# Kernel optimization log

Hardware: AMD Instinct MI355X
Metric: run time of the kernel (lower is better)

Reference implementation:

```python
import jax, jax.numpy as jnp
import numpy as np

N_HEADS = 8
N_LSTM_LAYERS = 32
HID = 25  # LSTM hidden units == decoder seq_len
EPS = 1e-5


def _layernorm(x, g, b):
    m = x.mean(-1, keepdims=True)
    v = x.var(-1, keepdims=True)  # biased, as torch LayerNorm
    return (x - m) / jnp.sqrt(v + EPS) * g + b


def _mha(q_in, k_in, v_in, Wq, bq, Wk, bk, Wv, bv, Wo, bo):
    B, L, D = q_in.shape
    S = k_in.shape[1]
    E = D // N_HEADS
    q = (q_in @ Wq + bq).reshape(B, L, N_HEADS, E)
    k = (k_in @ Wk + bk).reshape(B, S, N_HEADS, E)
    v = (v_in @ Wv + bv).reshape(B, S, N_HEADS, E)
    scores = jnp.einsum('blhe,bshe->bhls', q, k) / jnp.sqrt(jnp.asarray(E, q.dtype))
    attn = jax.nn.softmax(scores, axis=-1)
    out = jnp.einsum('bhls,bshe->blhe', attn, v).reshape(B, L, D)
    return out @ Wo + bo


def _lstm_layer(inp, W_ih, W_hh, b_ih, b_hh):
    # inp: [B, T, F]; PyTorch gate order i, f, g, o
    B = inp.shape[0]
    h0 = jnp.zeros((B, HID), inp.dtype)
    c0 = jnp.zeros((B, HID), inp.dtype)
    bias = b_ih + b_hh

    def step(carry, x_t):
        h, c = carry
        gates = x_t @ W_ih.T + h @ W_hh.T + bias  # [B, 4H]
        i, f, g, o = jnp.split(gates, 4, axis=-1)
        c = jax.nn.sigmoid(f) * c + jax.nn.sigmoid(i) * jnp.tanh(g)
        h = jax.nn.sigmoid(o) * jnp.tanh(c)
        return (h, c), h

    xs = jnp.swapaxes(inp, 0, 1)  # [T, B, F]
    _, hs = jax.lax.scan(step, (h0, c0), xs)
    return jnp.swapaxes(hs, 0, 1)  # [B, T, H]


def _forward(x, cross,
             Wq_s, bq_s, Wk_s, bk_s, Wv_s, bv_s, Wo_s, bo_s,
             Wq_c, bq_c, Wk_c, bk_c, Wv_c, bv_c, Wo_c, bo_c,
             g1, b1, g2, b2, g3, b3,
             W_ih, W_hh, b_ih, b_hh, Wc, bc):
    x = x + _mha(x, x, x, Wq_s, bq_s, Wk_s, bk_s, Wv_s, bv_s, Wo_s, bo_s)
    x = _layernorm(x, g1, b1)
    x = x + _mha(x, cross, cross, Wq_c, bq_c, Wk_c, bk_c, Wv_c, bv_c, Wo_c, bo_c)
    x = _layernorm(x, g2, b2)
    # LSTM runs over the feature axis: [B, L=25, D=512] -> [B, T=512, F=25]
    y = jnp.swapaxes(x, 1, 2)
    for l in range(N_LSTM_LAYERS):
        y = _lstm_layer(y, W_ih[l], W_hh[l], b_ih[l], b_hh[l])
    # pointwise conv over channels (dim 1 of [B, 512, 25])
    final_y = jnp.einsum('oc,bcl->bol', Wc, y) + bc[None, :, None]
    final_y = jnp.swapaxes(final_y, 1, 2)  # [B, 25, 512]
    return _layernorm(x + final_y, g3, b3)


def setup_inputs() -> dict:
    key = jax.random.key(0)
    ks = jax.random.split(key, 24)
    B, L, S, D = 128, 25, 96, 512

    def rn(k, shape, scale=0.02):
        return jax.random.normal(k, shape, jnp.float32) * scale

    inp = {
        'x': jax.random.normal(ks[0], (B, L, D), jnp.float32),
        'cross': jax.random.normal(ks[1], (B, S, D), jnp.float32),
        'Wq_s': rn(ks[2], (D, D)), 'bq_s': jnp.zeros(D),
        'Wk_s': rn(ks[3], (D, D)), 'bk_s': jnp.zeros(D),
        'Wv_s': rn(ks[4], (D, D)), 'bv_s': jnp.zeros(D),
        'Wo_s': rn(ks[5], (D, D)), 'bo_s': jnp.zeros(D),
        'Wq_c': rn(ks[6], (D, D)), 'bq_c': jnp.zeros(D),
        'Wk_c': rn(ks[7], (D, D)), 'bk_c': jnp.zeros(D),
        'Wv_c': rn(ks[8], (D, D)), 'bv_c': jnp.zeros(D),
        'Wo_c': rn(ks[9], (D, D)), 'bo_c': jnp.zeros(D),
        'g1': jnp.ones(D), 'b1': jnp.zeros(D),
        'g2': jnp.ones(D), 'b2': jnp.zeros(D),
        'g3': jnp.ones(D), 'b3': jnp.zeros(D),
        'W_ih': rn(ks[10], (N_LSTM_LAYERS, 4 * HID, HID), 0.1),
        'W_hh': rn(ks[11], (N_LSTM_LAYERS, 4 * HID, HID), 0.1),
        'b_ih': jnp.zeros((N_LSTM_LAYERS, 4 * HID)),
        'b_hh': jnp.zeros((N_LSTM_LAYERS, 4 * HID)),
        'Wc': rn(ks[12], (D, D)), 'bc': jnp.zeros(D),
    }
    return inp


def reference(x, cross,
              Wq_s, bq_s, Wk_s, bk_s, Wv_s, bv_s, Wo_s, bo_s,
              Wq_c, bq_c, Wk_c, bk_c, Wv_c, bv_c, Wo_c, bo_c,
              g1, b1, g2, b2, g3, b3,
              W_ih, W_hh, b_ih, b_hh, Wc, bc):
    return _forward(x, cross,
                    Wq_s, bq_s, Wk_s, bk_s, Wv_s, bv_s, Wo_s, bo_s,
                    Wq_c, bq_c, Wk_c, bk_c, Wv_c, bv_c, Wo_c, bo_c,
                    g1, b1, g2, b2, g3, b3,
                    W_ih, W_hh, b_ih, b_hh, Wc, bc)
```

## Files before the change

kernel.cpp:

```cpp
#include <hip/hip_runtime.h>


#define EPS_LN 1e-5f

typedef _Float16 h2v __attribute__((ext_vector_type(2)));
typedef _Float16 h8v __attribute__((ext_vector_type(8)));
typedef float    f4v __attribute__((ext_vector_type(4)));

#if defined(__has_builtin)
#if __has_builtin(__builtin_amdgcn_fdot2)
#define HAVE_FDOT2 1
#endif
#endif

__device__ __forceinline__ float fdot2(h2v a, h2v b, float c) {
#ifdef HAVE_FDOT2
  return __builtin_amdgcn_fdot2(a, b, c, false);
#else
  return c + (float)a.x * (float)b.x + (float)a.y * (float)b.y;
#endif
}
__device__ __forceinline__ h2v bch2(unsigned int u) {
  return __builtin_bit_cast(h2v, u);
}

struct WPtrs { const float* p[9]; };

__global__ __launch_bounds__(256)
void prep_weights(WPtrs w, _Float16* __restrict__ dst) {
  __shared__ float tile[32][33];
  const int z = blockIdx.z;
  const int tx = threadIdx.x & 31, ty = threadIdx.x >> 5;
  const int bx = blockIdx.x, by = blockIdx.y;
  const float* in = w.p[z];
  _Float16* outp = dst + (size_t)z * 262144;
  if (z < 8) {
#pragma unroll
    for (int i = 0; i < 4; i++)
      tile[ty + i * 8][tx] = in[(size_t)(by * 32 + ty + i * 8) * 512 + bx * 32 + tx];
    __syncthreads();
#pragma unroll
    for (int i = 0; i < 4; i++)
      outp[(size_t)(bx * 32 + ty + i * 8) * 512 + by * 32 + tx] = (_Float16)tile[tx][ty + i * 8];
  } else {
#pragma unroll
    for (int i = 0; i < 4; i++) {
      size_t off = (size_t)(by * 32 + ty + i * 8) * 512 + bx * 32 + tx;
      outp[off] = (_Float16)in[off];
    }
  }
}

__global__ __launch_bounds__(256)
void gemm3(const float* __restrict__ A,
           const _Float16* __restrict__ BT0, const _Float16* __restrict__ BT1,
           const _Float16* __restrict__ BT2,
           const float* __restrict__ bias0, const float* __restrict__ bias1,
           const float* __restrict__ bias2,
           float* __restrict__ C0, float* __restrict__ C1, float* __restrict__ C2,
           int M) {
  __shared__ _Float16 Asld[64 * 40];
  __shared__ _Float16 Bsld[64 * 40];
  const int t = threadIdx.x;
  const int which = blockIdx.x >> 3;
  const int n0 = (blockIdx.x & 7) * 64;
  const int m0 = blockIdx.y * 64;
  const _Float16* BT = (which == 0) ? BT0 : (which == 1) ? BT1 : BT2;
  const float* bias  = (which == 0) ? bias0 : (which == 1) ? bias1 : bias2;
  float* C           = (which == 0) ? C0 : (which == 1) ? C1 : C2;

  const int r = t >> 2, q = t & 3;
  const int w = t >> 6;
  const int lane = t & 63;
  const int lm = lane & 15, q8 = lane >> 4;

  f4v acc[4] = {};
  for (int k0 = 0; k0 < 512; k0 += 32) {
    __syncthreads();
    float4 f0 = *(const float4*)&A[(size_t)(m0 + r) * 512 + k0 + q * 8];
    float4 f1 = *(const float4*)&A[(size_t)(m0 + r) * 512 + k0 + q * 8 + 4];
    h8v hvv = {(_Float16)f0.x, (_Float16)f0.y, (_Float16)f0.z, (_Float16)f0.w,
               (_Float16)f1.x, (_Float16)f1.y, (_Float16)f1.z, (_Float16)f1.w};
    *(h8v*)&Asld[r * 40 + q * 8] = hvv;
    *(uint4*)&Bsld[r * 40 + q * 8] = *(const uint4*)&BT[(size_t)(n0 + r) * 512 + k0 + q * 8];
    __syncthreads();
    h8v a = *(const h8v*)&Asld[(w * 16 + lm) * 40 + q8 * 8];
#pragma unroll
    for (int nt = 0; nt < 4; nt++) {
      h8v b = *(const h8v*)&Bsld[(nt * 16 + lm) * 40 + q8 * 8];
      acc[nt] = __builtin_amdgcn_mfma_f32_16x16x32_f16(a, b, acc[nt], 0, 0, 0);
    }
  }
#pragma unroll
  for (int nt = 0; nt < 4; nt++) {
    int gn = n0 + nt * 16 + lm;
    float bv = bias[gn];
#pragma unroll
    for (int rg = 0; rg < 4; rg++) {
      int gm = m0 + w * 16 + q8 * 4 + rg;
      C[(size_t)gm * 512 + gn] = acc[nt][rg] + bv;
    }
  }
}

template <int S>
__global__ __launch_bounds__(256)
void attn_scores(const float* __restrict__ Q, const float* __restrict__ K,
                 float* __restrict__ P) {
  __shared__ float Qs[25][64];
  __shared__ float Ks[S][65];
  const int h = blockIdx.x, b = blockIdx.y, t = threadIdx.x;
  for (int idx = t; idx < 25 * 64; idx += 256) {
    int l = idx >> 6, e = idx & 63;
    Qs[l][e] = Q[(b * 25 + l) * 512 + h * 64 + e];
  }
  for (int idx = t; idx < S * 64; idx += 256) {
    int s = idx >> 6, e = idx & 63;
    Ks[s][e] = K[(b * S + s) * 512 + h * 64 + e];
  }
  __syncthreads();
  float* Pb = P + (size_t)(b * 8 + h) * 25 * S;
  for (int idx = t; idx < 25 * S; idx += 256) {
    int l = idx / S, s = idx % S;
    float acc = 0.f;
#pragma unroll
    for (int e = 0; e < 64; e++) acc += Qs[l][e] * Ks[s][e];
    Pb[idx] = acc * 0.125f;
  }
}

template <int S>
__global__ __launch_bounds__(256)
void attn_out(const float* __restrict__ P, const float* __restrict__ V,
              float* __restrict__ O) {
  __shared__ float Ps[25][S];
  __shared__ float Vs[S][64];
  const int h = blockIdx.x, b = blockIdx.y, t = threadIdx.x;
  const float* Pb = P + (size_t)(b * 8 + h) * 25 * S;
  for (int idx = t; idx < 25 * S; idx += 256) Ps[idx / S][idx % S] = Pb[idx];
  for (int idx = t; idx < S * 64; idx += 256) {
    int s = idx >> 6, e = idx & 63;
    Vs[s][e] = V[(b * S + s) * 512 + h * 64 + e];
  }
  __syncthreads();
  if (t < 25) {
    float mx = -1e30f;
    for (int s = 0; s < S; s++) mx = fmaxf(mx, Ps[t][s]);
    float sum = 0.f;
    for (int s = 0; s < S; s++) { float p = __expf(Ps[t][s] - mx); Ps[t][s] = p; sum += p; }
    float r = 1.f / sum;
    for (int s = 0; s < S; s++) Ps[t][s] *= r;
  }
  __syncthreads();
  for (int idx = t; idx < 25 * 64; idx += 256) {
    int l = idx >> 6, e = idx & 63;
    float acc = 0.f;
    for (int s = 0; s < S; s++) acc += Ps[l][s] * Vs[s][e];
    O[(b * 25 + l) * 512 + h * 64 + e] = acc;
  }
}

__global__ __launch_bounds__(128)
void add_ln(const float* __restrict__ a, const float* __restrict__ b,
            const float* __restrict__ gw, const float* __restrict__ bw,
            float* __restrict__ out) {
  const int row = blockIdx.x, t = threadIdx.x;
  float4 va = ((const float4*)(a + (size_t)row * 512))[t];
  float4 vb = ((const float4*)(b + (size_t)row * 512))[t];
  float4 v = make_float4(va.x + vb.x, va.y + vb.y, va.z + vb.z, va.w + vb.w);
  float s = v.x + v.y + v.z + v.w;
  float q = v.x * v.x + v.y * v.y + v.z * v.z + v.w * v.w;
#pragma unroll
  for (int off = 32; off > 0; off >>= 1) {
    s += __shfl_down(s, off);
    q += __shfl_down(q, off);
  }
  __shared__ float red[4];
  if ((t & 63) == 0) { red[(t >> 6) * 2] = s; red[(t >> 6) * 2 + 1] = q; }
  __syncthreads();
  float S_ = red[0] + red[2], Q_ = red[1] + red[3];
  float mean = S_ * (1.f / 512.f);
  float var  = Q_ * (1.f / 512.f) - mean * mean;
  float inv  = rsqrtf(var + EPS_LN);
  float4 g4 = ((const float4*)gw)[t];
  float4 b4 = ((const float4*)bw)[t];
  float4 o;
  o.x = (v.x - mean) * inv * g4.x + b4.x;
  o.y = (v.y - mean) * inv * g4.y + b4.y;
  o.z = (v.z - mean) * inv * g4.z + b4.z;
  o.w = (v.w - mean) * inv * g4.w + b4.w;
  ((float4*)(out + (size_t)row * 512))[t] = o;
}

__global__ void transpose_dl(const float* __restrict__ in, float* __restrict__ outp) {
  const int b = blockIdx.x, t = threadIdx.x;
  for (int idx = t; idx < 25 * 512; idx += 256) {
    int l2 = idx / 512, c = idx % 512;
    outp[((size_t)b * 25 + l2) * 512 + c] = in[((size_t)b * 512 + c) * 25 + l2];
  }
}

__global__ __launch_bounds__(256)
void prep_x0r(const float* __restrict__ x2, _Float16* __restrict__ X0) {
  __shared__ float tile[25][516];
  const int b = blockIdx.x, t = threadIdx.x;
  for (int idx = t; idx < 25 * 512; idx += 256) {
    int u = idx >> 9, d = idx & 511;
    tile[u][d] = x2[((size_t)b * 25 + u) * 512 + d];
  }
  __syncthreads();
  for (int idx = t; idx < 512 * 32; idx += 256) {
    int d = idx >> 5, u = idx & 31;
    X0[((size_t)b * 512 + d) * 32 + u] = (u < 25) ? (_Float16)tile[u][d] : (_Float16)0.f;
  }
}

#define NLAY 32
#define NGRP 16
#define BGRP 8
#define CHT  8
#define NCHK 64
#define RSLOTS 64
#define RCHK (RSLOTS / CHT)
#define RLAY ((size_t)128 * RSLOTS * 32)

__device__ __forceinline__ int ld_rlx(int* p) {
  return __hip_atomic_load(p, __ATOMIC_RELAXED, __HIP_MEMORY_SCOPE_AGENT);
}
__device__ __forceinline__ void st_rlx(int* p, int v) {
  __hip_atomic_store(p, v, __ATOMIC_RELAXED, __HIP_MEMORY_SCOPE_AGENT);
}
__device__ __forceinline__ unsigned long long ldq_rlx(const unsigned long long* p) {
  return __hip_atomic_load(p, __ATOMIC_RELAXED, __HIP_MEMORY_SCOPE_AGENT);
}
__device__ __forceinline__ void sth_rlx(_Float16* p, _Float16 v) {
  __hip_atomic_store((unsigned short*)p, __builtin_bit_cast(unsigned short, v),
                     __ATOMIC_RELAXED, __HIP_MEMORY_SCOPE_AGENT);
}
__device__ __forceinline__ float tanh_fast(float x) {
  return 1.f - 2.f / (1.f + __expf(2.f * x));
}

__global__ __launch_bounds__(256) __attribute__((amdgpu_waves_per_eu(2, 2)))
void lstm_pipeline(const _Float16* __restrict__ X0, float* __restrict__ yout,
                   _Float16* __restrict__ ring, int* __restrict__ prod,
                   int* __restrict__ cons,
                   const float* __restrict__ Wih, const float* __restrict__ Whh,
                   const float* __restrict__ bih, const float* __restrict__ bhh) {
  const int l = blockIdx.x / NGRP;
  const int g = blockIdx.x % NGRP;
  const int t = threadIdx.x;
  const int u  = t & 31;
  const int bi = t >> 5;
  const bool active = (u < 25);

  __shared__ _Float16 xbuf[CHT][BGRP][32];
  __shared__ _Float16 hbuf[BGRP][32];

  h2v wih2[4][13], whh2[4][13];
  float bias_r[4];
  float c_reg = 0.f;
  {
    const int uc = active ? u : 24;
#pragma unroll
    for (int j = 0; j < 4; j++) {
      const float* wi = &Wih[((size_t)l * 100 + j * 25 + uc) * 25];
      const float* wh = &Whh[((size_t)l * 100 + j * 25 + uc) * 25];
#pragma unroll
      for (int k = 0; k < 13; k++) {
        float alo = wi[2 * k], ahi = (2 * k + 1 < 25) ? wi[2 * k + 1] : 0.f;
        float blo = wh[2 * k], bhi = (2 * k + 1 < 25) ? wh[2 * k + 1] : 0.f;
        wih2[j][k] = h2v{(_Float16)alo, (_Float16)ahi};
        whh2[j][k] = h2v{(_Float16)blo, (_Float16)bhi};
      }
      bias_r[j] = bih[l * 100 + j * 25 + uc] + bhh[l * 100 + j * 25 + uc];
    }
  }
  for (int idx = t; idx < BGRP * 32; idx += 256) (&hbuf[0][0])[idx] = (_Float16)0.f;
  __syncthreads();

  _Float16* ring_out = ring + (size_t)l * RLAY
                       + ((size_t)(g * BGRP + bi) * RSLOTS) * 32 + u;
  float* yout_out = yout + ((size_t)(g * BGRP + bi) * 512) * 25 + u;

  const int s_tc = t >> 5, s_b2 = (t >> 2) & 7, s_seg = t & 3;

  for (int n = 0; n < NCHK; n++) {
    if (t == 0) {
      if (l > 0) {
        int* p = &prod[(l - 1) * NGRP + g];
        while (ld_rlx(p) < n + 1) __builtin_amdgcn_s_sleep(1);
      }
      if (l < NLAY - 1 && n >= RCHK) {
        int* p = &cons[(l + 1) * NGRP + g];
        while (ld_rlx(p) < n - RCHK + 1) __builtin_amdgcn_s_sleep(1);
      }
    }
    __syncthreads();
    {
      const int tg = n * CHT + s_tc;
      if (l == 0) {
        const uint4* p = (const uint4*)(X0
            + (((size_t)(g * BGRP + s_b2) * 512) + tg) * 32 + s_seg * 8);
        *(uint4*)&xbuf[s_tc][s_b2][s_seg * 8] = *p;
      } else {
        const unsigned long long* p = (const unsigned long long*)(ring
            + (size_t)(l - 1) * RLAY
            + (((size_t)(g * BGRP + s_b2) * RSLOTS) + (tg & (RSLOTS - 1))) * 32
            + s_seg * 8);
        unsigned long long a = ldq_rlx(p);
        unsigned long long b = ldq_rlx(p + 1);
        *(uint4*)&xbuf[s_tc][s_b2][s_seg * 8] =
            make_uint4((unsigned)a, (unsigned)(a >> 32),
                       (unsigned)b, (unsigned)(b >> 32));
      }
    }
    __syncthreads();
    if (t == 0 && l > 0) st_rlx(&cons[l * NGRP + g], n + 1);

    float ax[CHT][4];
    if (active) {
#pragma unroll
      for (int tc = 0; tc < CHT; tc++) {
        const unsigned int* xr = (const unsigned int*)&xbuf[tc][bi][0];
        uint4 xa = *(const uint4*)(xr);
        uint4 xb = *(const uint4*)(xr + 4);
        uint4 xc = *(const uint4*)(xr + 8);
        unsigned int xd = xr[12];
        h2v xk[13] = {bch2(xa.x), bch2(xa.y), bch2(xa.z), bch2(xa.w),
                      bch2(xb.x), bch2(xb.y), bch2(xb.z), bch2(xb.w),
                      bch2(xc.x), bch2(xc.y), bch2(xc.z), bch2(xc.w),
                      bch2(xd)};
        float a0 = bias_r[0], a1 = bias_r[1], a2 = bias_r[2], a3 = bias_r[3];
#pragma unroll
        for (int k = 0; k < 13; k++) {
          a0 = fdot2(wih2[0][k], xk[k], a0);
          a1 = fdot2(wih2[1][k], xk[k], a1);
          a2 = fdot2(wih2[2][k], xk[k], a2);
          a3 = fdot2(wih2[3][k], xk[k], a3);
        }
        ax[tc][0] = a0; ax[tc][1] = a1; ax[tc][2] = a2; ax[tc][3] = a3;
      }
    }

#pragma unroll
    for (int tc = 0; tc < CHT; tc++) {
      const int tg = n * CHT + tc;
      if (active) {
        const unsigned int* hr = (const unsigned int*)&hbuf[bi][0];
        uint4 ha = *(const uint4*)(hr);
        uint4 hb = *(const uint4*)(hr + 4);
        uint4 hc = *(const uint4*)(hr + 8);
        unsigned int hd = hr[12];
        h2v hk[13] = {bch2(ha.x), bch2(ha.y), bch2(ha.z), bch2(ha.w),
                      bch2(hb.x), bch2(hb.y), bch2(hb.z), bch2(hb.w),
                      bch2(hc.x), bch2(hc.y), bch2(hc.z), bch2(hc.w),
                      bch2(hd)};
        float a0 = ax[tc][0], a1 = ax[tc][1], a2 = ax[tc][2], a3 = ax[tc][3];
#pragma unroll
        for (int k = 0; k < 13; k++) {
          a0 = fdot2(whh2[0][k], hk[k], a0);
          a1 = fdot2(whh2[1][k], hk[k], a1);
          a2 = fdot2(whh2[2][k], hk[k], a2);
          a3 = fdot2(whh2[3][k], hk[k], a3);
        }
        float si = 1.f / (1.f + __expf(-a0));
        float sf = 1.f / (1.f + __expf(-a1));
        float so = 1.f / (1.f + __expf(-a3));
        c_reg = sf * c_reg + si * tanh_fast(a2);
        float h = so * tanh_fast(c_reg);
        _Float16 h16 = (_Float16)h;
        hbuf[bi][u] = h16;
        if (l == NLAY - 1)
          yout_out[(size_t)tg * 25] = h;
        else
          sth_rlx(ring_out + (size_t)(tg & (RSLOTS - 1)) * 32, h16);
      }
    }
    asm volatile("s_waitcnt vmcnt(0)" ::: "memory");
    __syncthreads();
    if (t == 0 && l < NLAY - 1) st_rlx(&prod[l * NGRP + g], n + 1);
  }
}

extern "C" void kernel_launch(void* const* d_in, const int* in_sizes, int n_in,
                              void* d_out, int out_size, void* d_ws, size_t ws_size,
                              hipStream_t stream) {
  const float* x     = (const float*)d_in[0];
  const float* cross = (const float*)d_in[1];
  const float* Wq_s = (const float*)d_in[2];  const float* bq_s = (const float*)d_in[3];
  const float* Wk_s = (const float*)d_in[4];  const float* bk_s = (const float*)d_in[5];
  const float* Wv_s = (const float*)d_in[6];  const float* bv_s = (const float*)d_in[7];
  const float* Wo_s = (const float*)d_in[8];  const float* bo_s = (const float*)d_in[9];
  const float* Wq_c = (const float*)d_in[10]; const float* bq_c = (const float*)d_in[11];
  const float* Wk_c = (const float*)d_in[12]; const float* bk_c = (const float*)d_in[13];
  const float* Wv_c = (const float*)d_in[14]; const float* bv_c = (const float*)d_in[15];
  const float* Wo_c = (const float*)d_in[16]; const float* bo_c = (const float*)d_in[17];
  const float* g1 = (const float*)d_in[18]; const float* b1 = (const float*)d_in[19];
  const float* g2 = (const float*)d_in[20]; const float* b2 = (const float*)d_in[21];
  const float* g3 = (const float*)d_in[22]; const float* b3 = (const float*)d_in[23];
  const float* Wih = (const float*)d_in[24];
  const float* Whh = (const float*)d_in[25];
  const float* bih = (const float*)d_in[26];
  const float* bhh = (const float*)d_in[27];
  const float* Wc  = (const float*)d_in[28]; const float* bc = (const float*)d_in[29];
  float* out = (float*)d_out;
  float* ws  = (float*)d_ws;

  constexpr size_t A  = 1638400;
  constexpr size_t C6 = 6291456;
  float* x1    = ws;
  float* Qc    = ws + A;
  float* Qs    = ws + 2 * A;
  float* Ks    = ws + 3 * A;
  float* Vs    = ws + 4 * A;
  float* attns = ws + 5 * A;
  float* tmp   = ws + 6 * A;
  float* Ps    = ws + 7 * A;
  float* Kc    = ws + 2 * A;
  float* Vc    = ws + 2 * A + C6;
  float* attnc = ws + 2 * A + 2 * C6;
  float* Pc    = attnc + A;
  float* tmp2  = ws + 6 * A;
  float* x2    = ws + 3 * A;
  _Float16* X0b  = (_Float16*)(ws + 4 * A);
  float*    youtb = ws + 5 * A;
  _Float16* ringb = (_Float16*)(ws + 6 * A);
  float* ytb   = ws + 2 * A;
  float* fy    = ws + 5 * A;
  _Float16* WTall = (_Float16*)(ws + 20000000);
  int* ctr = (int*)(ws + 21179648);

  dim3 blk(256);
  WPtrs wpq;
  wpq.p[0] = Wq_s; wpq.p[1] = Wk_s; wpq.p[2] = Wv_s; wpq.p[3] = Wo_s;
  wpq.p[4] = Wq_c; wpq.p[5] = Wk_c; wpq.p[6] = Wv_c; wpq.p[7] = Wo_c;
  wpq.p[8] = Wc;
  prep_weights<<<dim3(16, 16, 9), blk, 0, stream>>>(wpq, WTall);
  hipMemsetAsync(ctr, 0, 1024 * sizeof(int), stream);
  _Float16* WT[9];
  for (int i = 0; i < 9; i++) WT[i] = WTall + (size_t)i * 262144;

  gemm3<<<dim3(24, 50), blk, 0, stream>>>(x, WT[0], WT[1], WT[2],
                                          bq_s, bk_s, bv_s, Qs, Ks, Vs, 3200);
  attn_scores<25><<<dim3(8, 128), blk, 0, stream>>>(Qs, Ks, Ps);
  attn_out<25><<<dim3(8, 128), blk, 0, stream>>>(Ps, Vs, attns);
  gemm3<<<dim3(8, 50), blk, 0, stream>>>(attns, WT[3], WT[3], WT[3],
                                         bo_s, bo_s, bo_s, tmp, tmp, tmp, 3200);
  add_ln<<<3200, 128, 0, stream>>>(x, tmp, g1, b1, x1);
  gemm3<<<dim3(8, 50), blk, 0, stream>>>(x1, WT[4], WT[4], WT[4],
                                         bq_c, bq_c, bq_c, Qc, Qc, Qc, 3200);
  gemm3<<<dim3(16, 192), blk, 0, stream>>>(cross, WT[5], WT[6], WT[6],
                                           bk_c, bv_c, bv_c, Kc, Vc, Vc, 12288);
  attn_scores<96><<<dim3(8, 128), blk, 0, stream>>>(Qc, Kc, Pc);
  attn_out<96><<<dim3(8, 128), blk, 0, stream>>>(Pc, Vc, attnc);
  gemm3<<<dim3(8, 50), blk, 0, stream>>>(attnc, WT[7], WT[7], WT[7],
                                         bo_c, bo_c, bo_c, tmp2, tmp2, tmp2, 3200);
  add_ln<<<3200, 128, 0, stream>>>(x1, tmp2, g2, b2, x2);
  prep_x0r<<<128, 256, 0, stream>>>(x2, X0b);
  lstm_pipeline<<<NLAY * NGRP, 256, 0, stream>>>(X0b, youtb, ringb, ctr, ctr + 512,
                                                 Wih, Whh, bih, bhh);
  transpose_dl<<<128, 256, 0, stream>>>(youtb, ytb);
  gemm3<<<dim3(8, 50), blk, 0, stream>>>(ytb, WT[8], WT[8], WT[8],
                                         bc, bc, bc, fy, fy, fy, 3200);
  add_ln<<<3200, 128, 0, stream>>>(x2, fy, g3, b3, out);
}
```

Measured before the change: 1.045 ms.

## Double-buffer LSTM input chunks and prefetch next chunk during recurrence

Adds a second shared xbuf and issues the global/ring load for chunk n+1 before the sequential recurrence of chunk n, storing it to the other buffer afterwards. Producer/consumer flag polling is split: flags are read early and spins happen only if not yet ready, so the wait for the upstream layer overlaps the input projection. The goal is to hide inter-layer ring load latency and the handshake behind compute in the pipelined multi-layer LSTM. In exchange it adds a barrier per chunk, and the cons signalling changes to advance one chunk earlier, which could affect ring-slot safety.

```diff
diff --git a/kernel.cpp b/kernel.cpp
--- a/kernel.cpp
+++ b/kernel.cpp
@@ -254,7 +254,7 @@
   const int bi = t >> 5;
   const bool active = (u < 25);
 
-  __shared__ _Float16 xbuf[CHT][BGRP][32];
+  __shared__ _Float16 xbuf[2][CHT][BGRP][32];
   __shared__ _Float16 hbuf[BGRP][32];
 
   h2v wih2[4][13], whh2[4][13];
@@ -277,7 +277,6 @@
     }
   }
   for (int idx = t; idx < BGRP * 32; idx += 256) (&hbuf[0][0])[idx] = (_Float16)0.f;
-  __syncthreads();
 
   _Float16* ring_out = ring + (size_t)l * RLAY
                        + ((size_t)(g * BGRP + bi) * RSLOTS) * 32 + u;
@@ -285,44 +284,53 @@
 
   const int s_tc = t >> 5, s_b2 = (t >> 2) & 7, s_seg = t & 3;
 
+  int* prodp     = prod + (l - 1) * NGRP + g;
+  int* prod_self = prod + l * NGRP + g;
+  int* cons_self = cons + l * NGRP + g;
+  int* cons_up   = cons + (l + 1) * NGRP + g;
+
+  auto ldchunk = [&](int m) -> uint4 {
+    const int tg = m * CHT + s_tc;
+    if (l == 0) {
+      return *(const uint4*)(X0
+          + (((size_t)(g * BGRP + s_b2) * 512) + tg) * 32 + s_seg * 8);
+    } else {
+      const unsigned long long* p = (const unsigned long long*)(ring
+          + (size_t)(l - 1) * RLAY
+          + (((size_t)(g * BGRP + s_b2) * RSLOTS) + (tg & (RSLOTS - 1))) * 32
+          + s_seg * 8);
+      unsigned long long a = ldq_rlx(p);
+      unsigned long long b = ldq_rlx(p + 1);
+      return make_uint4((unsigned)a, (unsigned)(a >> 32),
+                        (unsigned)b, (unsigned)(b >> 32));
+    }
+  };
+
+  if (t == 0 && l > 0) {
+    while (ld_rlx(prodp) < 1) __builtin_amdgcn_s_sleep(1);
+  }
+  __syncthreads();
+  {
+    uint4 v0 = ldchunk(0);
+    *(uint4*)&xbuf[0][s_tc][s_b2][s_seg * 8] = v0;
+  }
+  __syncthreads();
+  if (t == 0 && l > 0) st_rlx(cons_self, 1);
+
+  int cur = 0;
   for (int n = 0; n < NCHK; n++) {
+    int pv = 0x7fffffff, cv = 0x7fffffff;
     if (t == 0) {
-      if (l > 0) {
-        int* p = &prod[(l - 1) * NGRP + g];
-        while (ld_rlx(p) < n + 1) __builtin_amdgcn_s_sleep(1);
-      }
-      if (l < NLAY - 1 && n >= RCHK) {
-        int* p = &cons[(l + 1) * NGRP + g];
-        while (ld_rlx(p) < n - RCHK + 1) __builtin_amdgcn_s_sleep(1);
-      }
-    }
-    __syncthreads();
-    {
-      const int tg = n * CHT + s_tc;
-      if (l == 0) {
-        const uint4* p = (const uint4*)(X0
-            + (((size_t)(g * BGRP + s_b2) * 512) + tg) * 32 + s_seg * 8);
-        *(uint4*)&xbuf[s_tc][s_b2][s_seg * 8] = *p;
-      } else {
-        const unsigned long long* p = (const unsigned long long*)(ring
-            + (size_t)(l - 1) * RLAY
-            + (((size_t)(g * BGRP + s_b2) * RSLOTS) + (tg & (RSLOTS - 1))) * 32
-            + s_seg * 8);
-        unsigned long long a = ldq_rlx(p);
-        unsigned long long b = ldq_rlx(p + 1);
-        *(uint4*)&xbuf[s_tc][s_b2][s_seg * 8] =
-            make_uint4((unsigned)a, (unsigned)(a >> 32),
-                       (unsigned)b, (unsigned)(b >> 32));
-      }
-    }
-    __syncthreads();
-    if (t == 0 && l > 0) st_rlx(&cons[l * NGRP + g], n + 1);
+      if (l > 0 && n + 1 < NCHK) pv = ld_rlx(prodp);
+      if (l < NLAY - 1 && n >= RCHK) cv = ld_rlx(cons_up);
+    }
+    asm volatile("" : "+v"(pv), "+v"(cv));
 
     float ax[CHT][4];
     if (active) {
 #pragma unroll
       for (int tc = 0; tc < CHT; tc++) {
-        const unsigned int* xr = (const unsigned int*)&xbuf[tc][bi][0];
+        const unsigned int* xr = (const unsigned int*)&xbuf[cur][tc][bi][0];
         uint4 xa = *(const uint4*)(xr);
         uint4 xb = *(const uint4*)(xr + 4);
         uint4 xc = *(const uint4*)(xr + 8);
@@ -342,6 +350,20 @@
         ax[tc][0] = a0; ax[tc][1] = a1; ax[tc][2] = a2; ax[tc][3] = a3;
       }
     }
+
+    if (t == 0) {
+      if (l < NLAY - 1 && n >= RCHK && cv < n - RCHK + 1) {
+        while (ld_rlx(cons_up) < n - RCHK + 1) __builtin_amdgcn_s_sleep(1);
+      }
+      if (l > 0 && n + 1 < NCHK && pv < n + 2) {
+        while (ld_rlx(prodp) < n + 2) __builtin_amdgcn_s_sleep(1);
+      }
+    }
+    __syncthreads();
+
+    const bool havepf = (n + 1 < NCHK);
+    uint4 pf;
+    if (havepf) pf = ldchunk(n + 1);
 
 #pragma unroll
     for (int tc = 0; tc < CHT; tc++) {
@@ -379,7 +401,11 @@
     }
     asm volatile("s_waitcnt vmcnt(0)" ::: "memory");
     __syncthreads();
-    if (t == 0 && l < NLAY - 1) st_rlx(&prod[l * NGRP + g], n + 1);
+    if (t == 0 && l < NLAY - 1) st_rlx(prod_self, n + 1);
+    if (havepf) *(uint4*)&xbuf[cur ^ 1][s_tc][s_b2][s_seg * 8] = pf;
+    __syncthreads();
+    if (t == 0 && l > 0 && havepf) st_rlx(cons_self, n + 2);
+    cur ^= 1;
   }
 }
 
```

Measured after the change: 1.139 ms. +9.0%, slower.

## Software-pipeline LSTM chunk loop: prefetch next input while running recurrent step

Applied to the files above, without the earlier changes.

Restructures the per-layer LSTM chunk loop so the global or ring load for chunk n is issued before the recurrent serial steps of chunk n-1 run, hiding load latency behind the recurrence. The input projection for chunk n is then computed after that data is staged into LDS. All threads now spin on the producer and consumer flags instead of only thread 0, which removes one barrier per chunk. The ring back-pressure condition and the flag publication are shifted by one chunk to match the new pipeline, which makes the handshake more delicate to get right.

```diff
diff --git a/kernel.cpp b/kernel.cpp
--- a/kernel.cpp
+++ b/kernel.cpp
@@ -285,40 +285,14 @@
 
   const int s_tc = t >> 5, s_b2 = (t >> 2) & 7, s_seg = t & 3;
 
-  for (int n = 0; n < NCHK; n++) {
-    if (t == 0) {
-      if (l > 0) {
-        int* p = &prod[(l - 1) * NGRP + g];
-        while (ld_rlx(p) < n + 1) __builtin_amdgcn_s_sleep(1);
-      }
-      if (l < NLAY - 1 && n >= RCHK) {
-        int* p = &cons[(l + 1) * NGRP + g];
-        while (ld_rlx(p) < n - RCHK + 1) __builtin_amdgcn_s_sleep(1);
-      }
-    }
-    __syncthreads();
-    {
-      const int tg = n * CHT + s_tc;
-      if (l == 0) {
-        const uint4* p = (const uint4*)(X0
-            + (((size_t)(g * BGRP + s_b2) * 512) + tg) * 32 + s_seg * 8);
-        *(uint4*)&xbuf[s_tc][s_b2][s_seg * 8] = *p;
-      } else {
-        const unsigned long long* p = (const unsigned long long*)(ring
-            + (size_t)(l - 1) * RLAY
-            + (((size_t)(g * BGRP + s_b2) * RSLOTS) + (tg & (RSLOTS - 1))) * 32
-            + s_seg * 8);
-        unsigned long long a = ldq_rlx(p);
-        unsigned long long b = ldq_rlx(p + 1);
-        *(uint4*)&xbuf[s_tc][s_b2][s_seg * 8] =
-            make_uint4((unsigned)a, (unsigned)(a >> 32),
-                       (unsigned)b, (unsigned)(b >> 32));
-      }
-    }
-    __syncthreads();
-    if (t == 0 && l > 0) st_rlx(&cons[l * NGRP + g], n + 1);
-
-    float ax[CHT][4];
+  int* prod_in   = prod + (l - 1) * NGRP + g;
+  int* prod_out  = prod + l * NGRP + g;
+  int* cons_self = cons + l * NGRP + g;
+  int* cons_up   = cons + (l + 1) * NGRP + g;
+
+  float ax[CHT][4];
+
+  auto do_ax = [&]() {
     if (active) {
 #pragma unroll
       for (int tc = 0; tc < CHT; tc++) {
@@ -342,10 +316,12 @@
         ax[tc][0] = a0; ax[tc][1] = a1; ax[tc][2] = a2; ax[tc][3] = a3;
       }
     }
-
+  };
+
+  auto do_serial = [&](int m) {
 #pragma unroll
     for (int tc = 0; tc < CHT; tc++) {
-      const int tg = n * CHT + tc;
+      const int tg = m * CHT + tc;
       if (active) {
         const unsigned int* hr = (const unsigned int*)&hbuf[bi][0];
         uint4 ha = *(const uint4*)(hr);
@@ -377,10 +353,57 @@
           sth_rlx(ring_out + (size_t)(tg & (RSLOTS - 1)) * 32, h16);
       }
     }
+  };
+
+  for (int n = 0; n < NCHK; n++) {
+    if (l > 0) {
+      while (ld_rlx(prod_in) < n + 1) __builtin_amdgcn_s_sleep(1);
+    }
+    if (l < NLAY - 1 && n > RCHK) {
+      while (ld_rlx(cons_up) < n - RCHK) __builtin_amdgcn_s_sleep(1);
+    }
+    asm volatile("" ::: "memory");
+
+    uint4 pf;
+    {
+      const int tg = n * CHT + s_tc;
+      if (l == 0) {
+        pf = *(const uint4*)(X0
+            + (((size_t)(g * BGRP + s_b2) * 512) + tg) * 32 + s_seg * 8);
+      } else {
+        const unsigned long long* p = (const unsigned long long*)(ring
+            + (size_t)(l - 1) * RLAY
+            + (((size_t)(g * BGRP + s_b2) * RSLOTS) + (tg & (RSLOTS - 1))) * 32
+            + s_seg * 8);
+        unsigned long long a = ldq_rlx(p);
+        unsigned long long b = ldq_rlx(p + 1);
+        pf = make_uint4((unsigned)a, (unsigned)(a >> 32),
+                        (unsigned)b, (unsigned)(b >> 32));
+      }
+    }
+
+    if (n > 0) do_serial(n - 1);
+
     asm volatile("s_waitcnt vmcnt(0)" ::: "memory");
+    *(uint4*)&xbuf[s_tc][s_b2][s_seg * 8] = pf;
     __syncthreads();
-    if (t == 0 && l < NLAY - 1) st_rlx(&prod[l * NGRP + g], n + 1);
-  }
+    if (t == 0) {
+      if (l < NLAY - 1 && n > 0) st_rlx(prod_out, n);
+      if (l > 0) st_rlx(cons_self, n + 1);
+    }
+
+    do_ax();
+    __syncthreads();
+  }
+
+  if (l < NLAY - 1) {
+    while (ld_rlx(cons_up) < NCHK - RCHK) __builtin_amdgcn_s_sleep(1);
+  }
+  asm volatile("" ::: "memory");
+  do_serial(NCHK - 1);
+  asm volatile("s_waitcnt vmcnt(0)" ::: "memory");
+  __syncthreads();
+  if (t == 0 && l < NLAY - 1) st_rlx(prod_out, NCHK);
 }
 
 extern "C" void kernel_launch(void* const* d_in, const int* in_sizes, int n_in,
```

Result: slower. 1.088 ms (+4.1%).

## Split LSTM gate rows across 50 lanes per wave and double block count

Applied to the files above, without the earlier changes.

Each LSTM batch row now gets a full 64-lane wave, and the 100 gate rows are split across 50 lanes with two gates each. The forget and output activations are exchanged with shuffles, instead of one thread computing all four gates for its unit. Batch rows per block drop from 8 to 4, so there are twice as many blocks (32 layers x 32 groups), and waves_per_eu rises to 4 to fit them. This halves the serial dot-product chain per recurrent step. The cost is more blocks spinning on flags, a shuffle on the critical path, and tighter register limits.

```diff
diff --git a/kernel.cpp b/kernel.cpp
--- a/kernel.cpp
+++ b/kernel.cpp
@@ -216,8 +216,8 @@
 }
 
 #define NLAY 32
-#define NGRP 16
-#define BGRP 8
+#define NGRP 32
+#define BGRP 4
 #define CHT  8
 #define NCHK 64
 #define RSLOTS 64
@@ -241,7 +241,7 @@
   return 1.f - 2.f / (1.f + __expf(2.f * x));
 }
 
-__global__ __launch_bounds__(256) __attribute__((amdgpu_waves_per_eu(2, 2)))
+__global__ __launch_bounds__(256) __attribute__((amdgpu_waves_per_eu(4, 4)))
 void lstm_pipeline(const _Float16* __restrict__ X0, float* __restrict__ yout,
                    _Float16* __restrict__ ring, int* __restrict__ prod,
                    int* __restrict__ cons,
@@ -250,22 +250,24 @@
   const int l = blockIdx.x / NGRP;
   const int g = blockIdx.x % NGRP;
   const int t = threadIdx.x;
-  const int u  = t & 31;
-  const int bi = t >> 5;
-  const bool active = (u < 25);
+  const int lane = t & 63;
+  const int wv   = t >> 6;
+  const bool gate_lane = (lane < 50);
+  const bool unit_lane = (lane < 25);
 
   __shared__ _Float16 xbuf[CHT][BGRP][32];
   __shared__ _Float16 hbuf[BGRP][32];
 
-  h2v wih2[4][13], whh2[4][13];
-  float bias_r[4];
+  h2v wih2[2][13], whh2[2][13];
+  float bias_r[2];
   float c_reg = 0.f;
   {
-    const int uc = active ? u : 24;
-#pragma unroll
-    for (int j = 0; j < 4; j++) {
-      const float* wi = &Wih[((size_t)l * 100 + j * 25 + uc) * 25];
-      const float* wh = &Whh[((size_t)l * 100 + j * 25 + uc) * 25];
+    const int r0 = gate_lane ? lane : 49;
+#pragma unroll
+    for (int j = 0; j < 2; j++) {
+      const int row = r0 + j * 50;
+      const float* wi = &Wih[((size_t)l * 100 + row) * 25];
+      const float* wh = &Whh[((size_t)l * 100 + row) * 25];
 #pragma unroll
       for (int k = 0; k < 13; k++) {
         float alo = wi[2 * k], ahi = (2 * k + 1 < 25) ? wi[2 * k + 1] : 0.f;
@@ -273,56 +275,57 @@
         wih2[j][k] = h2v{(_Float16)alo, (_Float16)ahi};
         whh2[j][k] = h2v{(_Float16)blo, (_Float16)bhi};
       }
-      bias_r[j] = bih[l * 100 + j * 25 + uc] + bhh[l * 100 + j * 25 + uc];
+      bias_r[j] = bih[l * 100 + row] + bhh[l * 100 + row];
     }
   }
   for (int idx = t; idx < BGRP * 32; idx += 256) (&hbuf[0][0])[idx] = (_Float16)0.f;
   __syncthreads();
 
+  const int bglob = g * BGRP + wv;
   _Float16* ring_out = ring + (size_t)l * RLAY
-                       + ((size_t)(g * BGRP + bi) * RSLOTS) * 32 + u;
-  float* yout_out = yout + ((size_t)(g * BGRP + bi) * 512) * 25 + u;
-
-  const int s_tc = t >> 5, s_b2 = (t >> 2) & 7, s_seg = t & 3;
+                       + ((size_t)bglob * RSLOTS) * 32 + lane;
+  float* yout_out = yout + ((size_t)bglob * 512) * 25 + lane;
+
+  const int s_tc = t >> 5, s_b2 = (t >> 3) & 3, s_seg = t & 7;
+
+  int* prod_in   = prod + (l - 1) * NGRP + g;
+  int* prod_out  = prod + l * NGRP + g;
+  int* cons_self = cons + l * NGRP + g;
+  int* cons_up   = cons + (l + 1) * NGRP + g;
 
   for (int n = 0; n < NCHK; n++) {
     if (t == 0) {
       if (l > 0) {
-        int* p = &prod[(l - 1) * NGRP + g];
-        while (ld_rlx(p) < n + 1) __builtin_amdgcn_s_sleep(1);
+        while (ld_rlx(prod_in) < n + 1) __builtin_amdgcn_s_sleep(1);
       }
       if (l < NLAY - 1 && n >= RCHK) {
-        int* p = &cons[(l + 1) * NGRP + g];
-        while (ld_rlx(p) < n - RCHK + 1) __builtin_amdgcn_s_sleep(1);
+        while (ld_rlx(cons_up) < n - RCHK + 1) __builtin_amdgcn_s_sleep(1);
       }
     }
     __syncthreads();
     {
       const int tg = n * CHT + s_tc;
       if (l == 0) {
-        const uint4* p = (const uint4*)(X0
-            + (((size_t)(g * BGRP + s_b2) * 512) + tg) * 32 + s_seg * 8);
-        *(uint4*)&xbuf[s_tc][s_b2][s_seg * 8] = *p;
+        unsigned long long a = *(const unsigned long long*)(X0
+            + (((size_t)(g * BGRP + s_b2) * 512) + tg) * 32 + s_seg * 4);
+        *(unsigned long long*)&xbuf[s_tc][s_b2][s_seg * 4] = a;
       } else {
         const unsigned long long* p = (const unsigned long long*)(ring
             + (size_t)(l - 1) * RLAY
             + (((size_t)(g * BGRP + s_b2) * RSLOTS) + (tg & (RSLOTS - 1))) * 32
-            + s_seg * 8);
+            + s_seg * 4);
         unsigned long long a = ldq_rlx(p);
-        unsigned long long b = ldq_rlx(p + 1);
-        *(uint4*)&xbuf[s_tc][s_b2][s_seg * 8] =
-            make_uint4((unsigned)a, (unsigned)(a >> 32),
-                       (unsigned)b, (unsigned)(b >> 32));
-      }
-    }
-    __syncthreads();
-    if (t == 0 && l > 0) st_rlx(&cons[l * NGRP + g], n + 1);
-
-    float ax[CHT][4];
-    if (active) {
+        *(unsigned long long*)&xbuf[s_tc][s_b2][s_seg * 4] = a;
+      }
+    }
+    __syncthreads();
+    if (t == 0 && l > 0) st_rlx(cons_self, n + 1);
+
+    float ax[CHT][2];
+    if (gate_lane) {
 #pragma unroll
       for (int tc = 0; tc < CHT; tc++) {
-        const unsigned int* xr = (const unsigned int*)&xbuf[tc][bi][0];
+        const unsigned int* xr = (const unsigned int*)&xbuf[tc][wv][0];
         uint4 xa = *(const uint4*)(xr);
         uint4 xb = *(const uint4*)(xr + 4);
         uint4 xc = *(const uint4*)(xr + 8);
@@ -331,23 +334,22 @@
                       bch2(xb.x), bch2(xb.y), bch2(xb.z), bch2(xb.w),
                       bch2(xc.x), bch2(xc.y), bch2(xc.z), bch2(xc.w),
                       bch2(xd)};
-        float a0 = bias_r[0], a1 = bias_r[1], a2 = bias_r[2], a3 = bias_r[3];
+        float a0 = bias_r[0], a1 = bias_r[1];
 #pragma unroll
         for (int k = 0; k < 13; k++) {
           a0 = fdot2(wih2[0][k], xk[k], a0);
           a1 = fdot2(wih2[1][k], xk[k], a1);
-          a2 = fdot2(wih2[2][k], xk[k], a2);
-          a3 = fdot2(wih2[3][k], xk[k], a3);
         }
-        ax[tc][0] = a0; ax[tc][1] = a1; ax[tc][2] = a2; ax[tc][3] = a3;
+        ax[tc][0] = a0; ax[tc][1] = a1;
       }
     }
 
 #pragma unroll
     for (int tc = 0; tc < CHT; tc++) {
       const int tg = n * CHT + tc;
-      if (active) {
-        const unsigned int* hr = (const unsigned int*)&hbuf[bi][0];
+      float s0 = 0.f, sg1 = 0.f, th1 = 0.f;
+      if (gate_lane) {
+        const unsigned int* hr = (const unsigned int*)&hbuf[wv][0];
         uint4 ha = *(const uint4*)(hr);
         uint4 hb = *(const uint4*)(hr + 4);
         uint4 hc = *(const uint4*)(hr + 8);
@@ -356,21 +358,23 @@
                       bch2(hb.x), bch2(hb.y), bch2(hb.z), bch2(hb.w),
                       bch2(hc.x), bch2(hc.y), bch2(hc.z), bch2(hc.w),
                       bch2(hd)};
-        float a0 = ax[tc][0], a1 = ax[tc][1], a2 = ax[tc][2], a3 = ax[tc][3];
+        float a0 = ax[tc][0], a1 = ax[tc][1];
 #pragma unroll
         for (int k = 0; k < 13; k++) {
           a0 = fdot2(whh2[0][k], hk[k], a0);
           a1 = fdot2(whh2[1][k], hk[k], a1);
-          a2 = fdot2(whh2[2][k], hk[k], a2);
-          a3 = fdot2(whh2[3][k], hk[k], a3);
         }
-        float si = 1.f / (1.f + __expf(-a0));
-        float sf = 1.f / (1.f + __expf(-a1));
-        float so = 1.f / (1.f + __expf(-a3));
-        c_reg = sf * c_reg + si * tanh_fast(a2);
+        s0  = 1.f / (1.f + __expf(-a0));
+        sg1 = 1.f / (1.f + __expf(-a1));
+        th1 = tanh_fast(a1);
+      }
+      float sf = __shfl(s0,  lane + 25);
+      float so = __shfl(sg1, lane + 25);
+      if (unit_lane) {
+        c_reg = sf * c_reg + s0 * th1;
         float h = so * tanh_fast(c_reg);
         _Float16 h16 = (_Float16)h;
-        hbuf[bi][u] = h16;
+        hbuf[wv][lane] = h16;
         if (l == NLAY - 1)
           yout_out[(size_t)tg * 25] = h;
         else
@@ -379,7 +383,7 @@
     }
     asm volatile("s_waitcnt vmcnt(0)" ::: "memory");
     __syncthreads();
-    if (t == 0 && l < NLAY - 1) st_rlx(&prod[l * NGRP + g], n + 1);
+    if (t == 0 && l < NLAY - 1) st_rlx(prod_out, n + 1);
   }
 }
 
@@ -437,7 +441,7 @@
   wpq.p[4] = Wq_c; wpq.p[5] = Wk_c; wpq.p[6] = Wv_c; wpq.p[7] = Wo_c;
   wpq.p[8] = Wc;
   prep_weights<<<dim3(16, 16, 9), blk, 0, stream>>>(wpq, WTall);
-  hipMemsetAsync(ctr, 0, 1024 * sizeof(int), stream);
+  hipMemsetAsync(ctr, 0, 2048 * sizeof(int), stream);
   _Float16* WT[9];
   for (int i = 0; i < 9; i++) WT[i] = WTall + (size_t)i * 262144;
 
@@ -458,7 +462,7 @@
                                          bo_c, bo_c, bo_c, tmp2, tmp2, tmp2, 3200);
   add_ln<<<3200, 128, 0, stream>>>(x1, tmp2, g2, b2, x2);
   prep_x0r<<<128, 256, 0, stream>>>(x2, X0b);
-  lstm_pipeline<<<NLAY * NGRP, 256, 0, stream>>>(X0b, youtb, ringb, ctr, ctr + 512,
+  lstm_pipeline<<<NLAY * NGRP, 256, 0, stream>>>(X0b, youtb, ringb, ctr, ctr + 1024,
                                                  Wih, Whh, bih, bhh);
   transpose_dl<<<128, 256, 0, stream>>>(youtb, ytb);
   gemm3<<<dim3(8, 50), blk, 0, stream>>>(ytb, WT[8], WT[8], WT[8],
```

New measurement: 1.048 ms. Within noise of the previous version (+0.3%).
